# Performance work log

Measured on AMD Instinct MI355X. Metric: run time of the kernel, lower is better.

The kernel has to match this reference:

```python
import jax, jax.numpy as jnp
import numpy as np

N_NODES = 50000
N_EDGES = 1600000
D = 128


def setup_inputs() -> dict:
    key = jax.random.key(0)
    k1, k2, k3, k4 = jax.random.split(key, 4)
    x = jax.random.normal(k1, (N_NODES, D), dtype=jnp.float32)
    edge_index = jax.random.randint(k2, (2, N_EDGES), 0, N_NODES, dtype=jnp.int64)
    # Xavier-uniform-like W; B is zeros in torch init but use small random for grad coverage
    limit = float(np.sqrt(6.0 / (D + D)))
    W = jax.random.uniform(k3, (D, D), dtype=jnp.float32, minval=-limit, maxval=limit)
    B = jax.random.uniform(k4, (D, D), dtype=jnp.float32, minval=-limit, maxval=limit)
    return {"x": x, "edge_index": edge_index, "W": W, "B": B}


def reference(x, edge_index, W, B):
    sources = edge_index[0]
    destinations = edge_index[1]
    # gather messages from source nodes, scatter-add into destinations
    messages = x[sources]  # [E, D]
    aggregated = jax.ops.segment_sum(messages, destinations, num_segments=N_NODES)  # [N, D]
    deg = jax.ops.segment_sum(jnp.ones((N_EDGES,), dtype=x.dtype), destinations, num_segments=N_NODES)
    deg = jnp.where(deg == 0, jnp.asarray(1.0, dtype=x.dtype), deg)
    mean_msg = aggregated / deg[:, None]
    # update: messages @ W.T + x @ B.T
    return mean_msg @ W.T + x @ B.T
```

## Files before the change

### kernel.cpp

```cpp
#include <hip/hip_runtime.h>
#include <hip/hip_bf16.h>

#define NN 50000
#define NE 1600000
#define DD 128
#define NPB 64
#define NBK 782
#define MAXB 2560
#define CHUNK 8192
#define NCB 196
#define WS 136

typedef __attribute__((ext_vector_type(8))) short short8;
typedef __attribute__((ext_vector_type(4))) float f32x4;

__device__ inline unsigned short to_bf16(float v) {
    __hip_bfloat16 h = __float2bfloat16(v);
    return __builtin_bit_cast(unsigned short, h);
}

__global__ __launch_bounds__(512) void convscatter_k(const int* __restrict__ ei,
                                                     const float* __restrict__ x,
                                                     unsigned int* __restrict__ xb,
                                                     int* __restrict__ gcursor,
                                                     int* __restrict__ ebuf) {
    __shared__ int stg[CHUNK];
    __shared__ int h[NBK];
    __shared__ int lbase[NBK];
    __shared__ int gb[NBK];
    __shared__ int hcur[NBK];
    __shared__ int sc[512];
    const int t = threadIdx.x;
    const int e0 = blockIdx.x * CHUNK;
    const int ec = min(CHUNK, NE - e0);

    for (int i = t; i < NBK; i += 512) h[i] = 0;
    __syncthreads();

    unsigned int w2[16];
    #pragma unroll
    for (int u = 0; u < 16; ++u) {
        int i = u * 512 + t;
        if (i < ec) {
            int src = ei[e0 + i];
            int dst = ei[NE + e0 + i];
            int b = dst >> 6;
            w2[u] = ((unsigned)b << 22) | ((unsigned)src << 6) | (unsigned)(dst & 63);
            atomicAdd(&h[b], 1);
        } else w2[u] = 0xFFFFFFFFu;
    }

    {
        int gid = blockIdx.x * 512 + t;
        const int total4 = NN * DD / 4;
        for (int i = gid; i < total4; i += NCB * 512) {
            float4 v = ((const float4*)x)[i];
            unsigned int lo = (unsigned)to_bf16(v.x) | ((unsigned)to_bf16(v.y) << 16);
            unsigned int hi = (unsigned)to_bf16(v.z) | ((unsigned)to_bf16(v.w) << 16);
            ((uint2*)xb)[i] = make_uint2(lo, hi);
        }
    }
    __syncthreads();

    int b0 = 2 * t, b1 = 2 * t + 1;
    int h0 = (b0 < NBK) ? h[b0] : 0;
    int h1 = (b1 < NBK) ? h[b1] : 0;
    int v = h0 + h1;
    sc[t] = v;
    __syncthreads();
    #pragma unroll
    for (int o = 1; o < 512; o <<= 1) {
        int a = (t >= o) ? sc[t - o] : 0;
        __syncthreads();
        sc[t] += a;
        __syncthreads();
    }
    int excl = sc[t] - v;
    if (b0 < NBK) {
        lbase[b0] = excl; hcur[b0] = excl;
        gb[b0] = h0 ? b0 * MAXB + atomicAdd(&gcursor[b0], h0) : 0;
    }
    if (b1 < NBK) {
        lbase[b1] = excl + h0; hcur[b1] = excl + h0;
        gb[b1] = h1 ? b1 * MAXB + atomicAdd(&gcursor[b1], h1) : 0;
    }
    __syncthreads();

    #pragma unroll
    for (int u = 0; u < 16; ++u) {
        if (w2[u] != 0xFFFFFFFFu) {
            int b = w2[u] >> 22;
            int pos = atomicAdd(&hcur[b], 1);
            stg[pos] = (int)w2[u];
        }
    }
    __syncthreads();

    for (int i = t; i < ec; i += 512) {
        unsigned int w = (unsigned)stg[i];
        int b = w >> 22;
        ebuf[gb[b] + (i - lbase[b])] = (int)(w & 0x3FFFFFu);
    }
}

__global__ __launch_bounds__(512) void sortagg_k(const unsigned int* __restrict__ xb,
                                                 const int* __restrict__ ebuf,
                                                 const int* __restrict__ gcursor,
                                                 unsigned int* __restrict__ meanb) {
    __shared__ int stg[MAXB];
    __shared__ unsigned short srt[MAXB];
    __shared__ int cnt[NPB], cur[NPB], off[NPB + 1];
    const int b = blockIdx.x, t = threadIdx.x;
    const int n = gcursor[b];
    const int* __restrict__ slab = ebuf + (size_t)b * MAXB;
    for (int i = t; i < n; i += 512) stg[i] = slab[i];
    if (t < NPB) cnt[t] = 0;
    __syncthreads();
    for (int i = t; i < n; i += 512) atomicAdd(&cnt[stg[i] & 63], 1);
    __syncthreads();
    if (t < 64) {
        int v = cnt[t];
        int s = v;
        #pragma unroll
        for (int o = 1; o < 64; o <<= 1) {
            int u = __shfl_up(s, o);
            if (t >= o) s += u;
        }
        cur[t] = s - v;
        off[t] = s - v;
        if (t == 63) off[64] = s;
    }
    __syncthreads();
    for (int i = t; i < n; i += 512) {
        int w = stg[i];
        int pos = atomicAdd(&cur[w & 63], 1);
        srt[pos] = (unsigned short)(w >> 6);
    }
    __syncthreads();

    const int wv = t >> 6, lane = t & 63;
    #pragma unroll
    for (int q = 0; q < 8; ++q) {
        int ln = wv + q * 8;
        int s0 = off[ln], s1 = off[ln + 1];
        float ax[8], ay[8];
        #pragma unroll
        for (int k = 0; k < 8; ++k) { ax[k] = 0.f; ay[k] = 0.f; }
        int i = s0;
        for (; i + 8 <= s1; i += 8) {
            unsigned int u[8];
            #pragma unroll
            for (int k = 0; k < 8; ++k) u[k] = xb[(size_t)srt[i + k] * 64 + lane];
            #pragma unroll
            for (int k = 0; k < 8; ++k) {
                ax[k] += __uint_as_float(u[k] << 16);
                ay[k] += __uint_as_float(u[k] & 0xffff0000u);
            }
        }
        for (; i < s1; ++i) {
            unsigned int u0 = xb[(size_t)srt[i] * 64 + lane];
            ax[0] += __uint_as_float(u0 << 16);
            ay[0] += __uint_as_float(u0 & 0xffff0000u);
        }
        int node = b * NPB + ln;
        if (node < NN) {
            float sx = ((ax[0] + ax[1]) + (ax[2] + ax[3])) + ((ax[4] + ax[5]) + (ax[6] + ax[7]));
            float sy = ((ay[0] + ay[1]) + (ay[2] + ay[3])) + ((ay[4] + ay[5]) + (ay[6] + ay[7]));
            float inv = 1.0f / fmaxf((float)(s1 - s0), 1.0f);
            meanb[(size_t)node * 64 + lane] =
                (unsigned)to_bf16(sx * inv) | ((unsigned)to_bf16(sy * inv) << 16);
        }
    }
}

__global__ __launch_bounds__(256) void gemm_mfma_k(const unsigned short* __restrict__ meanb,
                                                   const float* __restrict__ x,
                                                   const float* __restrict__ W,
                                                   const float* __restrict__ Bm,
                                                   float* __restrict__ out) {
    __shared__ unsigned short Wt[DD * WS];
    __shared__ unsigned short Bt[DD * WS];
    const int tid = threadIdx.x;
    #pragma unroll
    for (int it = 0; it < 16; ++it) {
        int idx = it * 256 + tid;
        int n = idx >> 5;
        int k0 = (idx & 31) * 4;
        float4 w4 = ((const float4*)W)[idx];
        float4 b4 = ((const float4*)Bm)[idx];
        ushort4 wp, bp;
        wp.x = to_bf16(w4.x); wp.y = to_bf16(w4.y); wp.z = to_bf16(w4.z); wp.w = to_bf16(w4.w);
        bp.x = to_bf16(b4.x); bp.y = to_bf16(b4.y); bp.z = to_bf16(b4.z); bp.w = to_bf16(b4.w);
        *(ushort4*)&Wt[n * WS + k0] = wp;
        *(ushort4*)&Bt[n * WS + k0] = bp;
    }
    __syncthreads();

    const int wave = tid >> 6;
    const int lane = tid & 63;
    const int m = lane & 15;
    const int quad = lane >> 4;
    const int rowA = min(blockIdx.x * 64 + wave * 16 + m, NN - 1);

    f32x4 acc[8];
    #pragma unroll
    for (int nt = 0; nt < 8; ++nt) acc[nt] = (f32x4){0.f, 0.f, 0.f, 0.f};

    #pragma unroll
    for (int t = 0; t < 4; ++t) {
        const int k8 = t * 32 + quad * 8;
        short8 mf = *(const short8*)&meanb[(size_t)rowA * DD + k8];
        float xv[8];
        {
            const float4* xq = (const float4*)&x[(size_t)rowA * DD + k8];
            float4 b0 = xq[0], b1 = xq[1];
            xv[0] = b0.x; xv[1] = b0.y; xv[2] = b0.z; xv[3] = b0.w;
            xv[4] = b1.x; xv[5] = b1.y; xv[6] = b1.z; xv[7] = b1.w;
        }
        short8 xh, xl;
        #pragma unroll
        for (int j = 0; j < 8; ++j) {
            unsigned short g = to_bf16(xv[j]);
            xh[j] = (short)g;
            xl[j] = (short)to_bf16(xv[j] - __uint_as_float((unsigned)g << 16));
        }
        #pragma unroll
        for (int nt = 0; nt < 8; ++nt) {
            int nrow = nt * 16 + m;
            short8 wf = *(const short8*)&Wt[nrow * WS + k8];
            short8 bf = *(const short8*)&Bt[nrow * WS + k8];
            acc[nt] = __builtin_amdgcn_mfma_f32_16x16x32_bf16(xl, bf, acc[nt], 0, 0, 0);
            acc[nt] = __builtin_amdgcn_mfma_f32_16x16x32_bf16(mf, wf, acc[nt], 0, 0, 0);
            acc[nt] = __builtin_amdgcn_mfma_f32_16x16x32_bf16(xh, bf, acc[nt], 0, 0, 0);
        }
    }

    const int rowD0 = blockIdx.x * 64 + wave * 16 + quad * 4;
    #pragma unroll
    for (int nt = 0; nt < 8; ++nt) {
        #pragma unroll
        for (int r = 0; r < 4; ++r) {
            int row = rowD0 + r;
            if (row < NN) out[(size_t)row * DD + nt * 16 + m] = acc[nt][r];
        }
    }
}

extern "C" void kernel_launch(void* const* d_in, const int* in_sizes, int n_in,
                              void* d_out, int out_size, void* d_ws, size_t ws_size,
                              hipStream_t stream) {
    const float* x  = (const float*)d_in[0];
    const int*   ei = (const int*)d_in[1];
    const float* W  = (const float*)d_in[2];
    const float* Bm = (const float*)d_in[3];
    float* out = (float*)d_out;

    unsigned int* meanb = (unsigned int*)d_ws;
    unsigned int* xb    = meanb + (size_t)NN * 64;
    int* ebuf     = (int*)(xb + (size_t)NN * 64);
    int* gcursor  = ebuf + (size_t)NBK * MAXB;

    hipMemsetAsync(gcursor, 0, NBK * sizeof(int), stream);
    convscatter_k<<<NCB, 512, 0, stream>>>(ei, x, xb, gcursor, ebuf);
    sortagg_k<<<NBK, 512, 0, stream>>>(xb, ebuf, gcursor, meanb);
    gemm_mfma_k<<<(NN + 63) / 64, 256, 0, stream>>>((const unsigned short*)meanb, x, W, Bm, out);
}
```

Measured before the change: 175.0 us.

## Store gathered node features as FP8 and use 1024-thread scatter blocks

Converts the x copy used for neighbour gathers from bf16 to packed FP8 (4 values per 32-bit word), halving the bytes read per edge during aggregation. The aggregation kernel now has each half-wave handle alternate edges and combines the halves with a cross-lane shuffle. The scatter kernel moves to 1024-thread blocks with smaller chunks, so each thread scans one bucket instead of two. FP8 quantisation of x adds much more error to the mean messages, which may exceed the accuracy tolerance.

After: 154.4 us. 1.13x faster.

```diff
diff --git a/kernel.cpp b/kernel.cpp
--- a/kernel.cpp
+++ b/kernel.cpp
@@ -7,8 +7,8 @@
 #define NPB 64
 #define NBK 782
 #define MAXB 2560
-#define CHUNK 8192
-#define NCB 196
+#define CHUNK 6144
+#define NCB 261
 #define WS 136
 
 typedef __attribute__((ext_vector_type(8))) short short8;
@@ -19,28 +19,28 @@
     return __builtin_bit_cast(unsigned short, h);
 }
 
-__global__ __launch_bounds__(512) void convscatter_k(const int* __restrict__ ei,
-                                                     const float* __restrict__ x,
-                                                     unsigned int* __restrict__ xb,
-                                                     int* __restrict__ gcursor,
-                                                     int* __restrict__ ebuf) {
+__global__ __launch_bounds__(1024) void convscatter_k(const int* __restrict__ ei,
+                                                      const float* __restrict__ x,
+                                                      unsigned int* __restrict__ xb,
+                                                      int* __restrict__ gcursor,
+                                                      int* __restrict__ ebuf) {
     __shared__ int stg[CHUNK];
     __shared__ int h[NBK];
     __shared__ int lbase[NBK];
     __shared__ int gb[NBK];
     __shared__ int hcur[NBK];
-    __shared__ int sc[512];
+    __shared__ int sc[1024];
     const int t = threadIdx.x;
     const int e0 = blockIdx.x * CHUNK;
     const int ec = min(CHUNK, NE - e0);
 
-    for (int i = t; i < NBK; i += 512) h[i] = 0;
-    __syncthreads();
-
-    unsigned int w2[16];
-    #pragma unroll
-    for (int u = 0; u < 16; ++u) {
-        int i = u * 512 + t;
+    for (int i = t; i < NBK; i += 1024) h[i] = 0;
+    __syncthreads();
+
+    unsigned int w2[6];
+    #pragma unroll
+    for (int u = 0; u < 6; ++u) {
+        int i = u * 1024 + t;
         if (i < ec) {
             int src = ei[e0 + i];
             int dst = ei[NE + e0 + i];
@@ -51,43 +51,37 @@
     }
 
     {
-        int gid = blockIdx.x * 512 + t;
+        int gid = blockIdx.x * 1024 + t;
         const int total4 = NN * DD / 4;
-        for (int i = gid; i < total4; i += NCB * 512) {
+        for (int i = gid; i < total4; i += NCB * 1024) {
             float4 v = ((const float4*)x)[i];
-            unsigned int lo = (unsigned)to_bf16(v.x) | ((unsigned)to_bf16(v.y) << 16);
-            unsigned int hi = (unsigned)to_bf16(v.z) | ((unsigned)to_bf16(v.w) << 16);
-            ((uint2*)xb)[i] = make_uint2(lo, hi);
-        }
-    }
-    __syncthreads();
-
-    int b0 = 2 * t, b1 = 2 * t + 1;
-    int h0 = (b0 < NBK) ? h[b0] : 0;
-    int h1 = (b1 < NBK) ? h[b1] : 0;
-    int v = h0 + h1;
+            int p = __builtin_amdgcn_cvt_pk_fp8_f32(v.x, v.y, 0, false);
+            p = __builtin_amdgcn_cvt_pk_fp8_f32(v.z, v.w, p, true);
+            xb[i] = (unsigned)p;
+        }
+    }
+    __syncthreads();
+
+    int v = (t < NBK) ? h[t] : 0;
     sc[t] = v;
     __syncthreads();
     #pragma unroll
-    for (int o = 1; o < 512; o <<= 1) {
+    for (int o = 1; o < 1024; o <<= 1) {
         int a = (t >= o) ? sc[t - o] : 0;
         __syncthreads();
         sc[t] += a;
         __syncthreads();
     }
     int excl = sc[t] - v;
-    if (b0 < NBK) {
-        lbase[b0] = excl; hcur[b0] = excl;
-        gb[b0] = h0 ? b0 * MAXB + atomicAdd(&gcursor[b0], h0) : 0;
-    }
-    if (b1 < NBK) {
-        lbase[b1] = excl + h0; hcur[b1] = excl + h0;
-        gb[b1] = h1 ? b1 * MAXB + atomicAdd(&gcursor[b1], h1) : 0;
-    }
-    __syncthreads();
-
-    #pragma unroll
-    for (int u = 0; u < 16; ++u) {
+    if (t < NBK) {
+        lbase[t] = excl;
+        hcur[t] = excl;
+        gb[t] = v ? t * MAXB + atomicAdd(&gcursor[t], v) : 0;
+    }
+    __syncthreads();
+
+    #pragma unroll
+    for (int u = 0; u < 6; ++u) {
         if (w2[u] != 0xFFFFFFFFu) {
             int b = w2[u] >> 22;
             int pos = atomicAdd(&hcur[b], 1);
@@ -96,7 +90,7 @@
     }
     __syncthreads();
 
-    for (int i = t; i < ec; i += 512) {
+    for (int i = t; i < ec; i += 1024) {
         unsigned int w = (unsigned)stg[i];
         int b = w >> 22;
         ebuf[gb[b] + (i - lbase[b])] = (int)(w & 0x3FFFFFu);
@@ -139,36 +133,42 @@
     __syncthreads();
 
     const int wv = t >> 6, lane = t & 63;
+    const int half = lane >> 5, il = lane & 31;
     #pragma unroll
     for (int q = 0; q < 8; ++q) {
         int ln = wv + q * 8;
         int s0 = off[ln], s1 = off[ln + 1];
-        float ax[8], ay[8];
-        #pragma unroll
-        for (int k = 0; k < 8; ++k) { ax[k] = 0.f; ay[k] = 0.f; }
+        float a0 = 0.f, a1 = 0.f, a2 = 0.f, a3 = 0.f;
         int i = s0;
-        for (; i + 8 <= s1; i += 8) {
+        for (; i + 16 <= s1; i += 16) {
             unsigned int u[8];
             #pragma unroll
-            for (int k = 0; k < 8; ++k) u[k] = xb[(size_t)srt[i + k] * 64 + lane];
+            for (int k = 0; k < 8; ++k)
+                u[k] = xb[(size_t)srt[i + 2 * k + half] * 32 + il];
             #pragma unroll
             for (int k = 0; k < 8; ++k) {
-                ax[k] += __uint_as_float(u[k] << 16);
-                ay[k] += __uint_as_float(u[k] & 0xffff0000u);
+                auto lo = __builtin_amdgcn_cvt_pk_f32_fp8((int)u[k], false);
+                auto hi = __builtin_amdgcn_cvt_pk_f32_fp8((int)u[k], true);
+                a0 += lo[0]; a1 += lo[1]; a2 += hi[0]; a3 += hi[1];
             }
         }
-        for (; i < s1; ++i) {
-            unsigned int u0 = xb[(size_t)srt[i] * 64 + lane];
-            ax[0] += __uint_as_float(u0 << 16);
-            ay[0] += __uint_as_float(u0 & 0xffff0000u);
-        }
+        for (; i < s1; i += 2) {
+            int e = i + half;
+            unsigned int u = (e < s1) ? xb[(size_t)srt[e] * 32 + il] : 0u;
+            auto lo = __builtin_amdgcn_cvt_pk_f32_fp8((int)u, false);
+            auto hi = __builtin_amdgcn_cvt_pk_f32_fp8((int)u, true);
+            a0 += lo[0]; a1 += lo[1]; a2 += hi[0]; a3 += hi[1];
+        }
+        a0 += __shfl_xor(a0, 32);
+        a1 += __shfl_xor(a1, 32);
+        a2 += __shfl_xor(a2, 32);
+        a3 += __shfl_xor(a3, 32);
         int node = b * NPB + ln;
-        if (node < NN) {
-            float sx = ((ax[0] + ax[1]) + (ax[2] + ax[3])) + ((ax[4] + ax[5]) + (ax[6] + ax[7]));
-            float sy = ((ay[0] + ay[1]) + (ay[2] + ay[3])) + ((ay[4] + ay[5]) + (ay[6] + ay[7]));
+        if (half == 0 && node < NN) {
             float inv = 1.0f / fmaxf((float)(s1 - s0), 1.0f);
-            meanb[(size_t)node * 64 + lane] =
-                (unsigned)to_bf16(sx * inv) | ((unsigned)to_bf16(sy * inv) << 16);
+            unsigned lo = (unsigned)to_bf16(a0 * inv) | ((unsigned)to_bf16(a1 * inv) << 16);
+            unsigned hi = (unsigned)to_bf16(a2 * inv) | ((unsigned)to_bf16(a3 * inv) << 16);
+            ((uint2*)meanb)[(size_t)node * 32 + il] = make_uint2(lo, hi);
         }
     }
 }
@@ -257,11 +257,11 @@
 
     unsigned int* meanb = (unsigned int*)d_ws;
     unsigned int* xb    = meanb + (size_t)NN * 64;
-    int* ebuf     = (int*)(xb + (size_t)NN * 64);
+    int* ebuf     = (int*)(xb + (size_t)NN * 32);
     int* gcursor  = ebuf + (size_t)NBK * MAXB;
 
     hipMemsetAsync(gcursor, 0, NBK * sizeof(int), stream);
-    convscatter_k<<<NCB, 512, 0, stream>>>(ei, x, xb, gcursor, ebuf);
+    convscatter_k<<<NCB, 1024, 0, stream>>>(ei, x, xb, gcursor, ebuf);
     sortagg_k<<<NBK, 512, 0, stream>>>(xb, ebuf, gcursor, meanb);
     gemm_mfma_k<<<(NN + 63) / 64, 256, 0, stream>>>((const unsigned short*)meanb, x, W, Bm, out);
 }
```
